# Performance work log

Measured on AMD Instinct MI355X. Metric: run time of the kernel, lower is better.

## Reference

```python
import jax, jax.numpy as jnp
import numpy as np

B, S, E, H = 4, 2048, 1024, 16
D = E // H  # head_size = 64

def setup_inputs() -> dict:
    key = jax.random.key(0)
    k1, k2, k3 = jax.random.split(key, 3)
    x = jax.random.normal(k1, (B, S, E), dtype=jnp.float32)
    # torch Linear weight is (out,in); we store transposed (in,out) for x @ W
    w_attn = jax.random.normal(k2, (E, 3 * E), dtype=jnp.float32) * (1.0 / np.sqrt(E))
    w_proj = jax.random.normal(k3, (E, E), dtype=jnp.float32) * (1.0 / np.sqrt(E))
    return {"x": x, "w_attn": w_attn, "w_proj": w_proj}

def reference(x, w_attn, w_proj):
    b, s, e = x.shape
    qkv = x @ w_attn                      # (B,S,3E)
    q, k, v = jnp.split(qkv, 3, axis=2)
    # (B,S,H,D) -> (B,H,S,D)
    q = q.reshape(b, s, H, D).transpose(0, 2, 1, 3)
    k = k.reshape(b, s, H, D).transpose(0, 2, 1, 3)
    v = v.reshape(b, s, H, D).transpose(0, 2, 1, 3)
    scale = 1.0 / np.sqrt(D).astype(np.float32)
    att = jnp.einsum('bhqd,bhkd->bhqk', q, k) * scale  # (B,H,S,S)
    causal = jnp.tril(jnp.ones((s, s), dtype=bool))
    att = jnp.where(causal[None, None, :, :], att, jnp.float32(-jnp.inf))
    att = jax.nn.softmax(att, axis=-1)
    # dropout layers are identity in eval mode
    y = jnp.einsum('bhqk,bhkd->bhqd', att, v)          # (B,H,S,D)
    y = y.transpose(0, 2, 1, 3).reshape(b, s, e)       # (B,S,E)
    return y @ w_proj
```

## Files before the change

kernel.cpp:

```cpp
#include <hip/hip_runtime.h>
#include <hip/hip_bf16.h>
#include <cstdint>

typedef __attribute__((ext_vector_type(8))) short bf16x8;
typedef __attribute__((ext_vector_type(4))) short short4v;
typedef __attribute__((ext_vector_type(4))) float f32x4;

#define MFMA(a, b, c) __builtin_amdgcn_mfma_f32_16x16x32_bf16((a), (b), (c), 0, 0, 0)

__device__ __forceinline__ unsigned short f2bf(float f) {
  union { float f; unsigned int u; } v;
  v.f = f;
  unsigned int r = v.u + 0x7FFFu + ((v.u >> 16) & 1u);
  return (unsigned short)(r >> 16);
}

__device__ __forceinline__ unsigned short f2bf_ru(float f) {
  union { float f; unsigned int u; } v;
  v.f = f;
  return (unsigned short)((v.u + 0x8000u) >> 16);
}

__device__ __forceinline__ void async_cp16(const unsigned short* g, unsigned short* l) {
  __builtin_amdgcn_global_load_lds(
      (const __attribute__((address_space(1))) unsigned int*)g,
      (__attribute__((address_space(3))) unsigned int*)l, 16, 0, 0);
}

__global__ __launch_bounds__(256) void cvt_x(const float* __restrict__ in,
                                             unsigned short* __restrict__ out) {
  size_t i = ((size_t)blockIdx.x * 256 + threadIdx.x) * 8;
  float4 a = *(const float4*)(in + i);
  float4 b = *(const float4*)(in + i + 4);
  bf16x8 p;
  p[0] = (short)f2bf(a.x); p[1] = (short)f2bf(a.y);
  p[2] = (short)f2bf(a.z); p[3] = (short)f2bf(a.w);
  p[4] = (short)f2bf(b.x); p[5] = (short)f2bf(b.y);
  p[6] = (short)f2bf(b.z); p[7] = (short)f2bf(b.w);
  *(bf16x8*)(out + i) = p;
}

__global__ __launch_bounds__(256) void transpose_cvt(const float* __restrict__ in,
                                                     unsigned short* __restrict__ out,
                                                     int K, int N) {
  __shared__ float tile[64][65];
  int k0 = blockIdx.x * 64;
  int n0 = blockIdx.y * 64;
  int c = threadIdx.x & 63;
  int rb = threadIdx.x >> 6;
#pragma unroll
  for (int i = 0; i < 16; ++i) {
    int r = rb * 16 + i;
    tile[r][c] = in[(size_t)(k0 + r) * N + (n0 + c)];
  }
  __syncthreads();
#pragma unroll
  for (int i = 0; i < 16; ++i) {
    int r = rb * 16 + i;
    out[(size_t)(n0 + r) * K + (k0 + c)] = f2bf(tile[c][r]);
  }
}

__global__ __launch_bounds__(256) void gemm_qkv(const unsigned short* __restrict__ X,
                                                const unsigned short* __restrict__ WT,
                                                unsigned short* __restrict__ qb,
                                                unsigned short* __restrict__ kb,
                                                unsigned short* __restrict__ vt) {
  const int K = 1024;
  __shared__ unsigned short As[128 * 64];
  __shared__ unsigned short Bs[128 * 64];
  int t = threadIdx.x, lane = t & 63, w = t >> 6;
  int quad = lane >> 4, l15 = lane & 15;
  int sl7 = l15 & 7;
  int wm = (w >> 1) * 64, wn = (w & 1) * 64;
  int row0 = blockIdx.y * 128, col0 = blockIdx.x * 128;
  int srow = w * 8 + (lane >> 3);
  int schunk = (lane & 7) ^ (lane >> 3);
  const unsigned short* aSrc = X + (size_t)(row0 + srow) * K + schunk * 8;
  const unsigned short* bSrc = WT + (size_t)(col0 + srow) * K + schunk * 8;
  unsigned short* ldsA = &As[(w * 8) * 64];
  unsigned short* ldsB = &Bs[(w * 8) * 64];
  f32x4 zero4 = {0.f, 0.f, 0.f, 0.f};
  f32x4 acc[4][4];
#pragma unroll
  for (int i = 0; i < 4; ++i)
#pragma unroll
    for (int j = 0; j < 4; ++j) acc[i][j] = zero4;

  for (int k0 = 0; k0 < K; k0 += 64) {
    __syncthreads();
#pragma unroll
    for (int i = 0; i < 4; ++i)
      async_cp16(aSrc + (size_t)i * 32 * K + k0, ldsA + i * 32 * 64);
#pragma unroll
    for (int i = 0; i < 4; ++i)
      async_cp16(bSrc + (size_t)i * 32 * K + k0, ldsB + i * 32 * 64);
    __syncthreads();
#pragma unroll
    for (int h = 0; h < 2; ++h) {
      bf16x8 af[4], bfr[4];
#pragma unroll
      for (int mt = 0; mt < 4; ++mt)
        af[mt] = *(const bf16x8*)&As[(wm + mt * 16 + l15) * 64 +
                                     ((h * 4 + quad) ^ sl7) * 8];
#pragma unroll
      for (int nt = 0; nt < 4; ++nt)
        bfr[nt] = *(const bf16x8*)&Bs[(wn + nt * 16 + l15) * 64 +
                                      ((h * 4 + quad) ^ sl7) * 8];
#pragma unroll
      for (int mt = 0; mt < 4; ++mt)
#pragma unroll
        for (int nt = 0; nt < 4; ++nt)
          acc[mt][nt] = MFMA(af[mt], bfr[nt], acc[mt][nt]);
    }
  }

  const float qscale = 0.125f * 1.4426950408889634f;
#pragma unroll
  for (int mt = 0; mt < 4; ++mt) {
    int rix0 = row0 + wm + mt * 16 + quad * 4;
    int b = rix0 >> 11;
    int s0 = rix0 & 2047;
#pragma unroll
    for (int nt = 0; nt < 4; ++nt) {
      int c = col0 + wn + nt * 16 + l15;
      int which = c >> 10;
      int e = c & 1023;
      int h = e >> 6, d = e & 63;
      size_t bh = (size_t)b * 16 + h;
      if (which == 2) {
        short4v pv;
#pragma unroll
        for (int r = 0; r < 4; ++r) pv[r] = (short)f2bf(acc[mt][nt][r]);
        *(short4v*)(vt + (bh * 64 + d) * 2048 + s0) = pv;
      } else {
        unsigned short* dst = (which == 0) ? qb : kb;
        float sc = (which == 0) ? qscale : 1.0f;
#pragma unroll
        for (int r = 0; r < 4; ++r)
          dst[(bh * 2048 + (s0 + r)) * 64 + d] = f2bf(acc[mt][nt][r] * sc);
      }
    }
  }
}

__global__ __launch_bounds__(256, 2) void flash_attn(const unsigned short* __restrict__ qb,
                                                     const unsigned short* __restrict__ kb,
                                                     const unsigned short* __restrict__ vt,
                                                     unsigned short* __restrict__ yb) {
  __shared__ unsigned short P[4][16 * 68];
  int idx = blockIdx.x;
  int p = idx >> 6;
  int sub = idx & 63;
  int bh = (sub & 7) * 8 + (sub >> 3);
  int t = threadIdx.x, lane = t & 63, w = t >> 6;
  int quad = lane >> 4, l15 = lane & 15;
  unsigned short* Pw = P[w];
  f32x4 zero4 = {0.f, 0.f, 0.f, 0.f};
  bf16x8 ones;
#pragma unroll
  for (int i = 0; i < 8; ++i) ones[i] = (short)0x3F80;
  int b = bh >> 4, h = bh & 15;
  const unsigned short* Kb = kb + (size_t)bh * (2048 * 64);
  const unsigned short* Vb = vt + (size_t)bh * (64 * 2048);

  for (int seg = 0; seg < 2; ++seg) {
    int qt = seg ? p : (15 - p);
    int qrow0 = qt * 128 + w * 32;
    int ktmax = (qrow0 + 31) >> 6;

    bf16x8 aq0[2], aq1[2];
#pragma unroll
    for (int s = 0; s < 2; ++s) {
      const unsigned short* Qp =
          qb + ((size_t)bh * 2048 + qrow0 + s * 16 + l15) * 64 + quad * 8;
      aq0[s] = *(const bf16x8*)Qp;
      aq1[s] = *(const bf16x8*)(Qp + 32);
    }
    f32x4 o[2][4], accl[2];
#pragma unroll
    for (int s = 0; s < 2; ++s) {
      accl[s] = zero4;
#pragma unroll
      for (int nt = 0; nt < 4; ++nt) o[s][nt] = zero4;
    }

    bf16x8 kA0[4], kA1[4], kB0[4], kB1[4];

#define LOADK(kb0, k0, k1)                                                    \
  do {                                                                        \
    _Pragma("unroll") for (int nt = 0; nt < 4; ++nt) {                        \
      const unsigned short* Kp =                                              \
          Kb + (size_t)((kb0) + nt * 16 + l15) * 64 + quad * 8;               \
      (k0)[nt] = *(const bf16x8*)Kp;                                          \
      (k1)[nt] = *(const bf16x8*)(Kp + 32);                                   \
    }                                                                         \
  } while (0)

#define COMPUTE(kbase_, k0, k1)                                               \
  do {                                                                        \
    int kbase = (kbase_);                                                     \
    bf16x8 vf0[4], vf1[4];                                                    \
    _Pragma("unroll") for (int nt = 0; nt < 4; ++nt) {                        \
      const unsigned short* Vp =                                              \
          Vb + (size_t)(nt * 16 + l15) * 2048 + kbase + quad * 8;             \
      vf0[nt] = *(const bf16x8*)Vp;                                           \
      vf1[nt] = *(const bf16x8*)(Vp + 32);                                    \
    }                                                                         \
    _Pragma("unroll") for (int s = 0; s < 2; ++s) {                           \
      int rowb = qrow0 + s * 16;                                              \
      if (kbase <= rowb + 15) {                             \
        f32x4 sv[4];                                                          \
        _Pragma("unroll") for (int nt = 0; nt < 4; ++nt) {                    \
          f32x4 z = zero4;                                                    \
          z = MFMA(aq0[s], (k0)[nt], z);                                      \
          z = MFMA(aq1[s], (k1)[nt], z);                                      \
          sv[nt] = z;                                                         \
        }                                                                     \
        if (kbase + 63 > rowb) {                \
          _Pragma("unroll") for (int nt = 0; nt < 4; ++nt) {                  \
            int col = kbase + nt * 16 + l15;                                  \
            _Pragma("unroll") for (int r = 0; r < 4; ++r)                     \
              if (col > rowb + quad * 4 + r) sv[nt][r] = -1e30f;              \
          }                                                                   \
        }                                                                     \
        _Pragma("unroll") for (int nt = 0; nt < 4; ++nt)                      \
          _Pragma("unroll") for (int r = 0; r < 4; ++r) {                     \
            float pv = __builtin_amdgcn_exp2f(sv[nt][r]);                     \
            Pw[(quad * 4 + r) * 68 + nt * 16 + l15] = f2bf_ru(pv);            \
          }                                                                   \
        bf16x8 ap0 = *(const bf16x8*)&Pw[l15 * 68 + quad * 8];                \
        bf16x8 ap1 = *(const bf16x8*)&Pw[l15 * 68 + 32 + quad * 8];           \
        accl[s] = MFMA(ap0, ones, accl[s]);                                   \
        accl[s] = MFMA(ap1, ones, accl[s]);                                   \
        _Pragma("unroll") for (int nt = 0; nt < 4; ++nt) {                    \
          o[s][nt] = MFMA(ap0, vf0[nt], o[s][nt]);                            \
          o[s][nt] = MFMA(ap1, vf1[nt], o[s][nt]);                            \
        }                                                                     \
      }                                                                       \
    }                                                                         \
  } while (0)

    LOADK(0, kA0, kA1);
    for (int kt = 0; kt <= ktmax; kt += 2) {
      if (kt + 1 <= ktmax) LOADK((kt + 1) * 64, kB0, kB1);
      COMPUTE(kt * 64, kA0, kA1);
      if (kt + 1 > ktmax) break;
      if (kt + 2 <= ktmax) LOADK((kt + 2) * 64, kA0, kA1);
      COMPUTE((kt + 1) * 64, kB0, kB1);
    }
#undef LOADK
#undef COMPUTE

#pragma unroll
    for (int s = 0; s < 2; ++s) {
      float inv[4];
#pragma unroll
      for (int r = 0; r < 4; ++r) inv[r] = 1.0f / accl[s][r];
#pragma unroll
      for (int nt = 0; nt < 4; ++nt) {
        int e = h * 64 + nt * 16 + l15;
#pragma unroll
        for (int r = 0; r < 4; ++r) {
          int srow_g = qrow0 + s * 16 + quad * 4 + r;
          yb[((size_t)b * 2048 + srow_g) * 1024 + e] = f2bf(o[s][nt][r] * inv[r]);
        }
      }
    }
  }
}

__global__ __launch_bounds__(256) void gemm_proj(const unsigned short* __restrict__ Y,
                                                 const unsigned short* __restrict__ WT,
                                                 float* __restrict__ out) {
  const int K = 1024;
  __shared__ unsigned short As[128 * 64];
  __shared__ unsigned short Bs[128 * 64];
  int t = threadIdx.x, lane = t & 63, w = t >> 6;
  int quad = lane >> 4, l15 = lane & 15;
  int sl7 = l15 & 7;
  int wm = (w >> 1) * 64, wn = (w & 1) * 64;
  int row0 = blockIdx.y * 128, col0 = blockIdx.x * 128;
  int srow = w * 8 + (lane >> 3);
  int schunk = (lane & 7) ^ (lane >> 3);
  const unsigned short* aSrc = Y + (size_t)(row0 + srow) * K + schunk * 8;
  const unsigned short* bSrc = WT + (size_t)(col0 + srow) * K + schunk * 8;
  unsigned short* ldsA = &As[(w * 8) * 64];
  unsigned short* ldsB = &Bs[(w * 8) * 64];
  f32x4 zero4 = {0.f, 0.f, 0.f, 0.f};
  f32x4 acc[4][4];
#pragma unroll
  for (int i = 0; i < 4; ++i)
#pragma unroll
    for (int j = 0; j < 4; ++j) acc[i][j] = zero4;

  for (int k0 = 0; k0 < K; k0 += 64) {
    __syncthreads();
#pragma unroll
    for (int i = 0; i < 4; ++i)
      async_cp16(aSrc + (size_t)i * 32 * K + k0, ldsA + i * 32 * 64);
#pragma unroll
    for (int i = 0; i < 4; ++i)
      async_cp16(bSrc + (size_t)i * 32 * K + k0, ldsB + i * 32 * 64);
    __syncthreads();
#pragma unroll
    for (int h = 0; h < 2; ++h) {
      bf16x8 af[4], bfr[4];
#pragma unroll
      for (int mt = 0; mt < 4; ++mt)
        af[mt] = *(const bf16x8*)&As[(wm + mt * 16 + l15) * 64 +
                                     ((h * 4 + quad) ^ sl7) * 8];
#pragma unroll
      for (int nt = 0; nt < 4; ++nt)
        bfr[nt] = *(const bf16x8*)&Bs[(wn + nt * 16 + l15) * 64 +
                                      ((h * 4 + quad) ^ sl7) * 8];
#pragma unroll
      for (int mt = 0; mt < 4; ++mt)
#pragma unroll
        for (int nt = 0; nt < 4; ++nt)
          acc[mt][nt] = MFMA(af[mt], bfr[nt], acc[mt][nt]);
    }
  }

#pragma unroll
  for (int mt = 0; mt < 4; ++mt) {
    int rix0 = row0 + wm + mt * 16 + quad * 4;
#pragma unroll
    for (int nt = 0; nt < 4; ++nt) {
      int c = col0 + wn + nt * 16 + l15;
#pragma unroll
      for (int r = 0; r < 4; ++r)
        out[(size_t)(rix0 + r) * 1024 + c] = acc[mt][nt][r];
    }
  }
}

extern "C" void kernel_launch(void* const* d_in, const int* in_sizes, int n_in,
                              void* d_out, int out_size, void* d_ws, size_t ws_size,
                              hipStream_t stream) {
  const float* x = (const float*)d_in[0];
  const float* w_attn = (const float*)d_in[1];
  const float* w_proj = (const float*)d_in[2];
  float* out = (float*)d_out;
  char* ws = (char*)d_ws;
  unsigned short* wT  = (unsigned short*)(ws + 0);
  unsigned short* wpT = (unsigned short*)(ws + 6291456);
  unsigned short* qb  = (unsigned short*)(ws + 8388608);
  unsigned short* kb  = (unsigned short*)(ws + 25165824);
  unsigned short* vt  = (unsigned short*)(ws + 41943040);
  unsigned short* xyb = (unsigned short*)(ws + 58720256);

  cvt_x<<<4096, 256, 0, stream>>>(x, xyb);
  transpose_cvt<<<dim3(16, 48), 256, 0, stream>>>(w_attn, wT, 1024, 3072);
  transpose_cvt<<<dim3(16, 16), 256, 0, stream>>>(w_proj, wpT, 1024, 1024);
  gemm_qkv<<<dim3(24, 64), 256, 0, stream>>>(xyb, wT, qb, kb, vt);
  flash_attn<<<dim3(512), 256, 0, stream>>>(qb, kb, vt, xyb);
  gemm_proj<<<dim3(8, 64), 256, 0, stream>>>(xyb, wpT, out);
}
```

Baseline: 302.7 us.

## Stage K tiles in shared LDS and keep P in registers via transposed QK^T

```diff
diff --git a/kernel.cpp b/kernel.cpp
--- a/kernel.cpp
+++ b/kernel.cpp
@@ -15,10 +15,10 @@
   return (unsigned short)(r >> 16);
 }
 
-__device__ __forceinline__ unsigned short f2bf_ru(float f) {
-  union { float f; unsigned int u; } v;
-  v.f = f;
-  return (unsigned short)((v.u + 0x8000u) >> 16);
+__device__ __forceinline__ unsigned int cvtpk(float lo, float hi) {
+  unsigned int r;
+  asm("v_cvt_pk_bf16_f32 %0, %1, %2" : "=v"(r) : "v"(lo), "v"(hi));
+  return r;
 }
 
 __device__ __forceinline__ void async_cp16(const unsigned short* g, unsigned short* l) {
@@ -148,26 +148,33 @@
                                                      const unsigned short* __restrict__ kb,
                                                      const unsigned short* __restrict__ vt,
                                                      unsigned short* __restrict__ yb) {
-  __shared__ unsigned short P[4][16 * 68];
+  __shared__ unsigned short Ks[2][64 * 64];
   int idx = blockIdx.x;
   int p = idx >> 6;
   int sub = idx & 63;
   int bh = (sub & 7) * 8 + (sub >> 3);
   int t = threadIdx.x, lane = t & 63, w = t >> 6;
   int quad = lane >> 4, l15 = lane & 15;
-  unsigned short* Pw = P[w];
   f32x4 zero4 = {0.f, 0.f, 0.f, 0.f};
   bf16x8 ones;
 #pragma unroll
   for (int i = 0; i < 8; ++i) ones[i] = (short)0x3F80;
   int b = bh >> 4, h = bh & 15;
-  const unsigned short* Kb = kb + (size_t)bh * (2048 * 64);
+
+  int srow_st = t >> 3;
+  int swz_st = (srow_st & 3) | (((srow_st >> 3) & 1) << 2);
+  int sslot = (t & 7) ^ swz_st;
+  const unsigned short* kp0 =
+      kb + ((size_t)bh * 2048 + srow_st) * 64 + sslot * 8;
   const unsigned short* Vb = vt + (size_t)bh * (64 * 2048);
+  int fbase = (l15 >> 2) * 8 + (l15 & 3);
+  int rslot0 = (quad ^ (l15 & 7)) * 8;
+  int rslot1 = ((quad ^ 4) ^ (l15 & 7)) * 8;
 
   for (int seg = 0; seg < 2; ++seg) {
     int qt = seg ? p : (15 - p);
     int qrow0 = qt * 128 + w * 32;
-    int ktmax = (qrow0 + 31) >> 6;
+    int ktmax = 2 * qt + 1;
 
     bf16x8 aq0[2], aq1[2];
 #pragma unroll
@@ -185,72 +192,97 @@
       for (int nt = 0; nt < 4; ++nt) o[s][nt] = zero4;
     }
 
-    bf16x8 kA0[4], kA1[4], kB0[4], kB1[4];
-
-#define LOADK(kb0, k0, k1)                                                    \
+    __syncthreads();
+    async_cp16(kp0, &Ks[0][t * 8]);
+    async_cp16(kp0 + 32 * 64, &Ks[0][2048 + t * 8]);
+    int cur = 0;
+
+    bf16x8 vA0[4], vA1[4], vB0[4], vB1[4];
+
+#define LOADV(KB, v0, v1)                                                     \
   do {                                                                        \
     _Pragma("unroll") for (int nt = 0; nt < 4; ++nt) {                        \
-      const unsigned short* Kp =                                              \
-          Kb + (size_t)((kb0) + nt * 16 + l15) * 64 + quad * 8;               \
-      (k0)[nt] = *(const bf16x8*)Kp;                                          \
-      (k1)[nt] = *(const bf16x8*)(Kp + 32);                                   \
+      const unsigned short* Vp =                                              \
+          Vb + (size_t)(nt * 16 + l15) * 2048 + (KB) + quad * 8;              \
+      (v0)[nt] = *(const bf16x8*)Vp;                                          \
+      (v1)[nt] = *(const bf16x8*)(Vp + 32);                                   \
     }                                                                         \
   } while (0)
 
-#define COMPUTE(kbase_, k0, k1)                                               \
+#define COMPUTE(KB, v0, v1)                                                   \
   do {                                                                        \
-    int kbase = (kbase_);                                                     \
-    bf16x8 vf0[4], vf1[4];                                                    \
+    int kbase = (KB);                                                         \
+    const unsigned short* Kc = &Ks[cur][0];                                   \
+    bf16x8 kf0[4], kf1[4];                                                    \
     _Pragma("unroll") for (int nt = 0; nt < 4; ++nt) {                        \
-      const unsigned short* Vp =                                              \
-          Vb + (size_t)(nt * 16 + l15) * 2048 + kbase + quad * 8;             \
-      vf0[nt] = *(const bf16x8*)Vp;                                           \
-      vf1[nt] = *(const bf16x8*)(Vp + 32);                                    \
+      int row = fbase + (nt & 1) * 4 + (nt >> 1) * 32;                        \
+      kf0[nt] = *(const bf16x8*)&Kc[row * 64 + rslot0];                       \
+      kf1[nt] = *(const bf16x8*)&Kc[row * 64 + rslot1];                       \
     }                                                                         \
     _Pragma("unroll") for (int s = 0; s < 2; ++s) {                           \
       int rowb = qrow0 + s * 16;                                              \
       if (kbase <= rowb + 15) {                             \
-        f32x4 sv[4];                                                          \
+        f32x4 pv4[4];                                                         \
         _Pragma("unroll") for (int nt = 0; nt < 4; ++nt) {                    \
           f32x4 z = zero4;                                                    \
-          z = MFMA(aq0[s], (k0)[nt], z);                                      \
-          z = MFMA(aq1[s], (k1)[nt], z);                                      \
-          sv[nt] = z;                                                         \
+          z = MFMA(kf0[nt], aq0[s], z);                                       \
+          z = MFMA(kf1[nt], aq1[s], z);                                       \
+          pv4[nt] = z;                                                        \
         }                                                                     \
-        if (kbase + 63 > rowb) {                \
+        if (kbase + 63 > rowb) {                    \
+          int qg = rowb + l15;                                                \
           _Pragma("unroll") for (int nt = 0; nt < 4; ++nt) {                  \
-            int col = kbase + nt * 16 + l15;                                  \
+            int colb = kbase + quad * 8 + (nt & 1) * 4 + ((nt >> 1) << 5);    \
             _Pragma("unroll") for (int r = 0; r < 4; ++r)                     \
-              if (col > rowb + quad * 4 + r) sv[nt][r] = -1e30f;              \
+              if (colb + r > qg) pv4[nt][r] = -1e30f;                         \
           }                                                                   \
         }                                                                     \
         _Pragma("unroll") for (int nt = 0; nt < 4; ++nt)                      \
-          _Pragma("unroll") for (int r = 0; r < 4; ++r) {                     \
-            float pv = __builtin_amdgcn_exp2f(sv[nt][r]);                     \
-            Pw[(quad * 4 + r) * 68 + nt * 16 + l15] = f2bf_ru(pv);            \
-          }                                                                   \
-        bf16x8 ap0 = *(const bf16x8*)&Pw[l15 * 68 + quad * 8];                \
-        bf16x8 ap1 = *(const bf16x8*)&Pw[l15 * 68 + 32 + quad * 8];           \
+          _Pragma("unroll") for (int r = 0; r < 4; ++r)                       \
+            pv4[nt][r] = __builtin_amdgcn_exp2f(pv4[nt][r]);                  \
+        union { unsigned int u[4]; bf16x8 v; } A0, A1;                        \
+        A0.u[0] = cvtpk(pv4[0][0], pv4[0][1]);                                \
+        A0.u[1] = cvtpk(pv4[0][2], pv4[0][3]);                                \
+        A0.u[2] = cvtpk(pv4[1][0], pv4[1][1]);                                \
+        A0.u[3] = cvtpk(pv4[1][2], pv4[1][3]);                                \
+        A1.u[0] = cvtpk(pv4[2][0], pv4[2][1]);                                \
+        A1.u[1] = cvtpk(pv4[2][2], pv4[2][3]);                                \
+        A1.u[2] = cvtpk(pv4[3][0], pv4[3][1]);                                \
+        A1.u[3] = cvtpk(pv4[3][2], pv4[3][3]);                                \
+        bf16x8 ap0 = A0.v, ap1 = A1.v;                                        \
         accl[s] = MFMA(ap0, ones, accl[s]);                                   \
         accl[s] = MFMA(ap1, ones, accl[s]);                                   \
         _Pragma("unroll") for (int nt = 0; nt < 4; ++nt) {                    \
-          o[s][nt] = MFMA(ap0, vf0[nt], o[s][nt]);                            \
-          o[s][nt] = MFMA(ap1, vf1[nt], o[s][nt]);                            \
+          o[s][nt] = MFMA(ap0, (v0)[nt], o[s][nt]);                           \
+          o[s][nt] = MFMA(ap1, (v1)[nt], o[s][nt]);                           \
         }                                                                     \
       }                                                                       \
     }                                                                         \
   } while (0)
 
-    LOADK(0, kA0, kA1);
+#define ITER(KT, cv0, cv1, nv0, nv1)                                          \
+  do {                                                                        \
+    int kb0 = (KT) * 64;                                                      \
+    __syncthreads();     \
+    if ((KT) < ktmax) {                                                       \
+      const unsigned short* nk = kp0 + (size_t)(kb0 + 64) * 64;               \
+      async_cp16(nk, &Ks[cur ^ 1][t * 8]);                                    \
+      async_cp16(nk + 32 * 64, &Ks[cur ^ 1][2048 + t * 8]);                   \
+    }                                                                         \
+    if ((KT) + 1 <= ktmax && kb0 + 64 <= qrow0 + 31) LOADV(kb0 + 64, nv0, nv1); \
+    if (kb0 <= qrow0 + 31) COMPUTE(kb0, cv0, cv1);                            \
+    cur ^= 1;                                                                 \
+  } while (0)
+
+    LOADV(0, vA0, vA1);
     for (int kt = 0; kt <= ktmax; kt += 2) {
-      if (kt + 1 <= ktmax) LOADK((kt + 1) * 64, kB0, kB1);
-      COMPUTE(kt * 64, kA0, kA1);
+      ITER(kt, vA0, vA1, vB0, vB1);
       if (kt + 1 > ktmax) break;
-      if (kt + 2 <= ktmax) LOADK((kt + 2) * 64, kA0, kA1);
-      COMPUTE((kt + 1) * 64, kB0, kB1);
-    }
-#undef LOADK
+      ITER(kt + 1, vB0, vB1, vA0, vA1);
+    }
+#undef ITER
 #undef COMPUTE
+#undef LOADV
 
 #pragma unroll
     for (int s = 0; s < 2; ++s) {
```

After: 249.8 us. 17.5% less time.
